# Kernel optimization log

Hardware: AMD Instinct MI355X
Metric: run time of the kernel (lower is better)

Reference implementation:

```python
import jax, jax.numpy as jnp
import numpy as np

L_LIST = [0, 1, 2, 3]
PAIRS = [(l1, l2) for l1 in L_LIST for l2 in L_LIST if l1 <= l2]
S, I, N = 8, 32, 8  # structures, atoms per structure, radial functions


def setup_inputs() -> dict:
    key = jax.random.key(0)
    inp = {}
    for l in L_LIST:
        key, k1, k2 = jax.random.split(key, 3)
        inp[f"c_in_l{l}"] = jax.random.normal(k1, (S, I, 2 * l + 1, N), dtype=jnp.float32)
        inp[f"c_tgt_l{l}"] = jax.random.normal(k2, (S, I, 2 * l + 1, N), dtype=jnp.float32)
    for (l1, l2) in PAIRS:
        key, k1 = jax.random.split(key)
        # overlap block stored pre-permuted: [S, i1, m1, n1, i2, m2, n2]
        inp[f"ovlp_l{l1}_l{l2}"] = jax.random.normal(
            k1, (S, I, 2 * l1 + 1, N, I, 2 * l2 + 1, N), dtype=jnp.float32)
    return inp


def _rho_loss(c_in, c_tgt, ovlp):
    # delta_coeffs = input - target, per (l) block (single species)
    d = {l: c_in[l] - c_tgt[l] for l in L_LIST}
    total = jnp.float32(0.0)
    for (l1, l2) in PAIRS:
        O = ovlp[(l1, l2)]
        # tensordot(c1, O, dims=3) over (i1, m1, n1), batched over structures s
        t = jnp.einsum('simn,simnjpq->sjpq', d[l1], O)
        # tensordot(t, c2, dims=3) over (i2, m2, n2), then sum over structures
        b = jnp.einsum('sjpq,sjpq->', t, d[l2])
        # diagonal blocks (l1==l2, a1==a2) counted once, off-diagonal twice
        total = total + (b if l1 == l2 else 2.0 * b)
    return total


def reference(c_in_l0, c_tgt_l0, c_in_l1, c_tgt_l1, c_in_l2, c_tgt_l2,
              c_in_l3, c_tgt_l3, ovlp_l0_l0, ovlp_l0_l1, ovlp_l0_l2,
              ovlp_l0_l3, ovlp_l1_l1, ovlp_l1_l2, ovlp_l1_l3, ovlp_l2_l2,
              ovlp_l2_l3, ovlp_l3_l3):
    c_in = {0: c_in_l0, 1: c_in_l1, 2: c_in_l2, 3: c_in_l3}
    c_tgt = {0: c_tgt_l0, 1: c_tgt_l1, 2: c_tgt_l2, 3: c_tgt_l3}
    ovlp = {(0, 0): ovlp_l0_l0, (0, 1): ovlp_l0_l1, (0, 2): ovlp_l0_l2,
            (0, 3): ovlp_l0_l3, (1, 1): ovlp_l1_l1, (1, 2): ovlp_l1_l2,
            (1, 3): ovlp_l1_l3, (2, 2): ovlp_l2_l2, (2, 3): ovlp_l2_l3,
            (3, 3): ovlp_l3_l3}
    return _rho_loss(c_in, c_tgt, ovlp)
```

## Files before the change

### kernel.cpp

```cpp
#include <hip/hip_runtime.h>


#define NUM_S 8

__device__ float g_d[32768];

__global__ __launch_bounds__(256) void compute_d_kernel(
    const float* __restrict__ ci0, const float* __restrict__ ct0,
    const float* __restrict__ ci1, const float* __restrict__ ct1,
    const float* __restrict__ ci2, const float* __restrict__ ct2,
    const float* __restrict__ ci3, const float* __restrict__ ct3) {
    const int t = blockIdx.x * 256 + threadIdx.x;
    float v;
    if (t < 2048)       v = ci0[t]         - ct0[t];
    else if (t < 8192)  v = ci1[t - 2048]  - ct1[t - 2048];
    else if (t < 18432) v = ci2[t - 8192]  - ct2[t - 8192];
    else                v = ci3[t - 18432] - ct3[t - 18432];
    g_d[t] = v;
}

#define NWAVES 8192

template <int K1, int K2, int W, int ROT>
__device__ __forceinline__ float pair_sum_rows(const float4* __restrict__ O4,
                                               const float* __restrict__ d1,
                                               const float* __restrict__ d2,
                                               int wid, int lane) {
    constexpr int C2q    = K2 / 4;
    constexpr int ROUNDS = C2q / 64;
    constexpr int NROWS  = NUM_S * K1;

    float ax = 0.f, ay = 0.f, az = 0.f, aw = 0.f;
    for (int t = (wid + ROT) & (NWAVES - 1); t < NROWS; t += NWAVES) {
        const int s = t / K1;
        const float4* __restrict__ o = O4 + (size_t)t * C2q + lane;
        const float4* __restrict__ v = (const float4*)(d2 + s * K2) + lane;

        float4 ov[ROUNDS], vv[ROUNDS];
#pragma unroll
        for (int j = 0; j < ROUNDS; ++j) ov[j] = o[j * 64];
#pragma unroll
        for (int j = 0; j < ROUNDS; ++j) vv[j] = v[j * 64];

        const float dd = d1[t];

        float dx = 0.f, dy = 0.f, dz = 0.f, dw = 0.f;
#pragma unroll
        for (int j = 0; j < ROUNDS; ++j) {
            dx = fmaf(ov[j].x, vv[j].x, dx);
            dy = fmaf(ov[j].y, vv[j].y, dy);
            dz = fmaf(ov[j].z, vv[j].z, dz);
            dw = fmaf(ov[j].w, vv[j].w, dw);
        }
        ax = fmaf(dd, dx, ax);
        ay = fmaf(dd, dy, ay);
        az = fmaf(dd, dz, az);
        aw = fmaf(dd, dw, aw);
    }
    return (float)W * ((ax + ay) + (az + aw));
}

__global__ __launch_bounds__(256) void rho_loss_kernel(
    const float* __restrict__ O00, const float* __restrict__ O01,
    const float* __restrict__ O02, const float* __restrict__ O03,
    const float* __restrict__ O11, const float* __restrict__ O12,
    const float* __restrict__ O13, const float* __restrict__ O22,
    const float* __restrict__ O23, const float* __restrict__ O33,
    float* __restrict__ out) {
    const int lane = threadIdx.x & 63;
    const int wid  = blockIdx.x * 4 + (threadIdx.x >> 6);

    const float* D0 = g_d;
    const float* D1 = g_d + 2048;
    const float* D2 = g_d + 8192;
    const float* D3 = g_d + 18432;

    float acc = 0.f;
    acc += pair_sum_rows< 256,  256, 1,    0>((const float4*)O00, D0, D0, wid, lane);
    acc += pair_sum_rows< 256,  768, 2,  819>((const float4*)O01, D0, D1, wid, lane);
    acc += pair_sum_rows< 256, 1280, 2, 1638>((const float4*)O02, D0, D2, wid, lane);
    acc += pair_sum_rows< 256, 1792, 2, 2457>((const float4*)O03, D0, D3, wid, lane);
    acc += pair_sum_rows< 768,  768, 1, 3276>((const float4*)O11, D1, D1, wid, lane);
    acc += pair_sum_rows< 768, 1280, 2, 4095>((const float4*)O12, D1, D2, wid, lane);
    acc += pair_sum_rows< 768, 1792, 2, 4914>((const float4*)O13, D1, D3, wid, lane);
    acc += pair_sum_rows<1280, 1280, 1, 5733>((const float4*)O22, D2, D2, wid, lane);
    acc += pair_sum_rows<1280, 1792, 2, 6552>((const float4*)O23, D2, D3, wid, lane);
    acc += pair_sum_rows<1792, 1792, 1, 7371>((const float4*)O33, D3, D3, wid, lane);

    for (int off = 32; off > 0; off >>= 1)
        acc += __shfl_down(acc, off, 64);

    __shared__ float wsum[4];
    const int lwid = threadIdx.x >> 6;
    if (lane == 0) wsum[lwid] = acc;
    __syncthreads();
    if (threadIdx.x == 0) {
        float s = wsum[0] + wsum[1] + wsum[2] + wsum[3];
        atomicAdd(out, s);
    }
}

extern "C" void kernel_launch(void* const* d_in, const int* in_sizes, int n_in,
                              void* d_out, int out_size, void* d_ws, size_t ws_size,
                              hipStream_t stream) {
    (void)in_sizes; (void)n_in; (void)d_ws; (void)ws_size; (void)out_size;

    const float* ci0 = (const float*)d_in[0];
    const float* ct0 = (const float*)d_in[1];
    const float* ci1 = (const float*)d_in[2];
    const float* ct1 = (const float*)d_in[3];
    const float* ci2 = (const float*)d_in[4];
    const float* ct2 = (const float*)d_in[5];
    const float* ci3 = (const float*)d_in[6];
    const float* ct3 = (const float*)d_in[7];
    const float* O00 = (const float*)d_in[8];
    const float* O01 = (const float*)d_in[9];
    const float* O02 = (const float*)d_in[10];
    const float* O03 = (const float*)d_in[11];
    const float* O11 = (const float*)d_in[12];
    const float* O12 = (const float*)d_in[13];
    const float* O13 = (const float*)d_in[14];
    const float* O22 = (const float*)d_in[15];
    const float* O23 = (const float*)d_in[16];
    const float* O33 = (const float*)d_in[17];

    hipMemsetAsync(d_out, 0, sizeof(float), stream);

    compute_d_kernel<<<128, 256, 0, stream>>>(ci0, ct0, ci1, ct1,
                                              ci2, ct2, ci3, ct3);

    rho_loss_kernel<<<2048, 256, 0, stream>>>(
        O00, O01, O02, O03, O11, O12, O13, O22, O23, O33, (float*)d_out);
}
```

Before: 344.5 us.

## Partition waves statically across overlap blocks and use nontemporal loads

Instead of every wave striding through all ten overlap blocks with rotated offsets, each wave now owns a contiguous range of rows within a single block. Wave counts are assigned in proportion to each block's byte size. Overlap loads use nontemporal hints so the streamed matrix does not pollute the cache. This is meant to improve load balance, make each wave's accesses contiguous, and remove per-block loop overhead. In exchange it hardcodes the wave partition, and the per-wave branch selects only one template instantiation.

```diff
diff --git a/kernel.cpp b/kernel.cpp
--- a/kernel.cpp
+++ b/kernel.cpp
@@ -2,6 +2,8 @@
 
 
 #define NUM_S 8
+
+typedef float vfloat4 __attribute__((ext_vector_type(4)));
 
 __device__ float g_d[32768];
 
@@ -19,26 +21,30 @@
     g_d[t] = v;
 }
 
-#define NWAVES 8192
-
-template <int K1, int K2, int W, int ROT>
-__device__ __forceinline__ float pair_sum_rows(const float4* __restrict__ O4,
-                                               const float* __restrict__ d1,
-                                               const float* __restrict__ d2,
-                                               int wid, int lane) {
+template <int K1, int K2, int W, int NWP>
+__device__ __forceinline__ float pair_rows(const float* __restrict__ O,
+                                           const float* __restrict__ d1,
+                                           const float* __restrict__ d2,
+                                           int lw, int lane) {
     constexpr int C2q    = K2 / 4;
     constexpr int ROUNDS = C2q / 64;
     constexpr int NROWS  = NUM_S * K1;
 
+    const int r_beg = (int)(((long long)lw * NROWS) / NWP);
+    const int r_end = (int)(((long long)(lw + 1) * NROWS) / NWP);
+
+    const vfloat4* __restrict__ O4 = (const vfloat4*)O;
+
     float ax = 0.f, ay = 0.f, az = 0.f, aw = 0.f;
-    for (int t = (wid + ROT) & (NWAVES - 1); t < NROWS; t += NWAVES) {
+    for (int t = r_beg; t < r_end; ++t) {
         const int s = t / K1;
-        const float4* __restrict__ o = O4 + (size_t)t * C2q + lane;
-        const float4* __restrict__ v = (const float4*)(d2 + s * K2) + lane;
+        const vfloat4* __restrict__ o = O4 + (size_t)t * C2q + lane;
+        const vfloat4* __restrict__ v = (const vfloat4*)(d2 + s * K2) + lane;
 
-        float4 ov[ROUNDS], vv[ROUNDS];
+        vfloat4 ov[ROUNDS], vv[ROUNDS];
 #pragma unroll
-        for (int j = 0; j < ROUNDS; ++j) ov[j] = o[j * 64];
+        for (int j = 0; j < ROUNDS; ++j)
+            ov[j] = __builtin_nontemporal_load(o + j * 64);
 #pragma unroll
         for (int j = 0; j < ROUNDS; ++j) vv[j] = v[j * 64];
 
@@ -75,17 +81,17 @@
     const float* D2 = g_d + 8192;
     const float* D3 = g_d + 18432;
 
-    float acc = 0.f;
-    acc += pair_sum_rows< 256,  256, 1,    0>((const float4*)O00, D0, D0, wid, lane);
-    acc += pair_sum_rows< 256,  768, 2,  819>((const float4*)O01, D0, D1, wid, lane);
-    acc += pair_sum_rows< 256, 1280, 2, 1638>((const float4*)O02, D0, D2, wid, lane);
-    acc += pair_sum_rows< 256, 1792, 2, 2457>((const float4*)O03, D0, D3, wid, lane);
-    acc += pair_sum_rows< 768,  768, 1, 3276>((const float4*)O11, D1, D1, wid, lane);
-    acc += pair_sum_rows< 768, 1280, 2, 4095>((const float4*)O12, D1, D2, wid, lane);
-    acc += pair_sum_rows< 768, 1792, 2, 4914>((const float4*)O13, D1, D3, wid, lane);
-    acc += pair_sum_rows<1280, 1280, 1, 5733>((const float4*)O22, D2, D2, wid, lane);
-    acc += pair_sum_rows<1280, 1792, 2, 6552>((const float4*)O23, D2, D3, wid, lane);
-    acc += pair_sum_rows<1792, 1792, 1, 7371>((const float4*)O33, D3, D3, wid, lane);
+    float acc;
+    if      (wid <   47) acc = pair_rows< 256,  256, 1,   47>(O00, D0, D0, wid,        lane);
+    else if (wid <  192) acc = pair_rows< 256,  768, 2,  145>(O01, D0, D1, wid -   47, lane);
+    else if (wid <  433) acc = pair_rows< 256, 1280, 2,  241>(O02, D0, D2, wid -  192, lane);
+    else if (wid <  770) acc = pair_rows< 256, 1792, 2,  337>(O03, D0, D3, wid -  433, lane);
+    else if (wid < 1204) acc = pair_rows< 768,  768, 1,  434>(O11, D1, D1, wid -  770, lane);
+    else if (wid < 1927) acc = pair_rows< 768, 1280, 2,  723>(O12, D1, D2, wid - 1204, lane);
+    else if (wid < 2939) acc = pair_rows< 768, 1792, 2, 1012>(O13, D1, D3, wid - 1927, lane);
+    else if (wid < 4144) acc = pair_rows<1280, 1280, 1, 1205>(O22, D2, D2, wid - 2939, lane);
+    else if (wid < 5831) acc = pair_rows<1280, 1792, 2, 1687>(O23, D2, D3, wid - 4144, lane);
+    else                 acc = pair_rows<1792, 1792, 1, 2361>(O33, D3, D3, wid - 5831, lane);
 
     for (int off = 32; off > 0; off >>= 1)
         acc += __shfl_down(acc, off, 64);
```

After: 321.4 us. 6.7% less time.
